# Kernel optimization log

Hardware: AMD Instinct MI355X
Metric: run time of the kernel (lower is better)

## Reference

```python
import jax, jax.numpy as jnp
import numpy as np

NUM_HEADS = 8
NUM_GROUPS = 32
EPS = 1e-5


def group_norm(x, gamma, beta):
    # x: [B, C, H, W]; normalize over (C//G, H, W) within each of G groups
    B, C, H, W = x.shape
    xg = x.reshape(B, NUM_GROUPS, C // NUM_GROUPS, H, W)
    mean = xg.mean(axis=(2, 3, 4), keepdims=True)
    var = xg.var(axis=(2, 3, 4), keepdims=True)
    xn = ((xg - mean) * jax.lax.rsqrt(var + EPS)).reshape(B, C, H, W)
    return xn * gamma[None, :, None, None] + beta[None, :, None, None]


def setup_inputs() -> dict:
    key = jax.random.key(0)
    ks = jax.random.split(key, 7)
    B, C, H, W = 16, 512, 32, 32
    x = jax.random.normal(ks[0], (B, C, H, W), dtype=jnp.float32)
    gamma = jnp.ones((C,), dtype=jnp.float32)
    beta = jnp.zeros((C,), dtype=jnp.float32)
    # 1x1 convs == per-pixel linear layers
    w_qkv = jax.random.normal(ks[1], (3 * C, C), dtype=jnp.float32) * (1.0 / np.sqrt(C))
    b_qkv = jax.random.normal(ks[2], (3 * C,), dtype=jnp.float32) * 0.02
    w_proj = jax.random.normal(ks[3], (C, C), dtype=jnp.float32) * (1.0 / np.sqrt(C))
    b_proj = jax.random.normal(ks[4], (C,), dtype=jnp.float32) * 0.02
    return {"x": x, "gamma": gamma, "beta": beta, "w_qkv": w_qkv,
            "b_qkv": b_qkv, "w_proj": w_proj, "b_proj": b_proj}


def reference(x, gamma, beta, w_qkv, b_qkv, w_proj, b_proj):
    B, C, H, W = x.shape
    nh = NUM_HEADS
    d = C // nh
    N = H * W
    h = group_norm(x, gamma, beta)
    # 1x1 conv: [B,C,H,W] x [3C,C] -> [B,3C,H,W]
    qkv = jnp.einsum('bchw,oc->bohw', h, w_qkv) + b_qkv[None, :, None, None]
    qkv = qkv.reshape(B, 3, nh, d, N)  # matches torch reshape(B,3,heads,d,HW)
    q, k, v = qkv[:, 0], qkv[:, 1], qkv[:, 2]
    scale = d ** (-0.5)
    attn = jnp.einsum('bhdn,bhdm->bhnm', q, k) * scale  # [B,h,N,N]
    attn = jax.nn.softmax(attn, axis=-1)
    out = jnp.einsum('bhnm,bhdm->bhdn', attn, v)  # [B,h,d,N]
    out = out.reshape(B, C, H, W)
    proj = jnp.einsum('bchw,oc->bohw', out, w_proj) + b_proj[None, :, None, None]
    return x + proj
```

## Files before the change

kernel.cpp:

```cpp
#include <hip/hip_runtime.h>
#include <cstddef>

#define B_  16
#define C_  512
#define N_  1024

typedef __attribute__((ext_vector_type(8))) __bf16 bf16x8;
typedef __attribute__((ext_vector_type(4))) float f32x4;
typedef __attribute__((ext_vector_type(4))) short s16x4;

__device__ __forceinline__ unsigned short f2bf(float x) {
  unsigned u = __float_as_uint(x);
  return (unsigned short)((u + 0x7fffu + ((u >> 16) & 1u)) >> 16);
}
__device__ __forceinline__ float bf2f(unsigned short h) {
  return __uint_as_float(((unsigned)h) << 16);
}

#define GLDS16(g, l)                                                            \
  __builtin_amdgcn_global_load_lds(                                             \
      (const __attribute__((address_space(1))) void*)(g),                       \
      (__attribute__((address_space(3))) void*)(l), 16, 0, 0)

__global__ __launch_bounds__(256) void prep_kernel(
    const float* __restrict__ wq, const float* __restrict__ wp,
    unsigned short* __restrict__ oq, unsigned short* __restrict__ op,
    const float* __restrict__ x, float* __restrict__ stats) {
  int tid = threadIdx.x;
  if (blockIdx.x < 1024) {
    int i = blockIdx.x * 256 + tid;
    const float4* src; unsigned short* dst; int off;
    if (i < 196608) { src = (const float4*)wq; dst = oq; off = i; }
    else            { src = (const float4*)wp; dst = op; off = i - 196608; }
    float4 v = src[off];
    union { unsigned short s[4]; ushort4 u; } o;
    o.s[0] = f2bf(v.x); o.s[1] = f2bf(v.y);
    o.s[2] = f2bf(v.z); o.s[3] = f2bf(v.w);
    *(ushort4*)(dst + (size_t)off * 4) = o.u;
    return;
  }
  int bg = blockIdx.x - 1024;
  int b = bg >> 5, g = bg & 31;
  const float4* x4 = (const float4*)(x + ((size_t)b * C_ + (size_t)g * 16) * N_);
  float sum = 0.f, sq = 0.f;
#pragma unroll
  for (int i = 0; i < 16; i++) {
    float4 v = x4[tid + i * 256];
    sum += v.x + v.y + v.z + v.w;
    sq  += v.x * v.x + v.y * v.y + v.z * v.z + v.w * v.w;
  }
#pragma unroll
  for (int off = 32; off > 0; off >>= 1) {
    sum += __shfl_down(sum, off, 64);
    sq  += __shfl_down(sq, off, 64);
  }
  __shared__ float sm[4], sv[4];
  int lane = tid & 63, w = tid >> 6;
  if (lane == 0) { sm[w] = sum; sv[w] = sq; }
  __syncthreads();
  if (tid == 0) {
    float s = sm[0] + sm[1] + sm[2] + sm[3];
    float q = sv[0] + sv[1] + sv[2] + sv[3];
    float mean = s * (1.f / 16384.f);
    float var  = q * (1.f / 16384.f) - mean * mean;
    stats[bg * 2]     = mean;
    stats[bg * 2 + 1] = rsqrtf(var + 1e-5f);
  }
}

__global__ __launch_bounds__(256) void gn_norm(
    const float* __restrict__ x, const float* __restrict__ gamma,
    const float* __restrict__ beta, const float* __restrict__ stats,
    unsigned short* __restrict__ hT) {
  __shared__ __align__(16) unsigned short T[64][72];

  const int bi = blockIdx.x;
  const int nq = bi & 3, g4 = (bi >> 2) & 7, b = bi >> 5;
  const int tid = threadIdx.x, lane = tid & 63, w = tid >> 6;
  const int c0 = g4 * 64, n0 = nq * 256;
  const int q = lane >> 4, n4 = lane & 15;

  const int gidx = b * 32 + g4 * 4 + w;
  const float mean = stats[gidx * 2], rstd = stats[gidx * 2 + 1];
  float ga[4], be[4];
#pragma unroll
  for (int ri = 0; ri < 4; ri++) {
    int c = w * 16 + q + ri * 4;
    ga[ri] = gamma[c0 + c] * rstd;
    be[ri] = beta[c0 + c] - mean * ga[ri];
  }

  const float* xb = x + ((size_t)b * C_ + c0) * N_ + n0;

#pragma unroll
  for (int s = 0; s < 4; s++) {
#pragma unroll
    for (int ri = 0; ri < 4; ri++) {
      int c = w * 16 + q + ri * 4;
      float4 v = *(const float4*)&xb[(size_t)c * N_ + s * 64 + n4 * 4];
      int csw = c ^ ((n4 & 3) << 4);
      T[n4 * 4 + 0][csw] = f2bf(v.x * ga[ri] + be[ri]);
      T[n4 * 4 + 1][csw] = f2bf(v.y * ga[ri] + be[ri]);
      T[n4 * 4 + 2][csw] = f2bf(v.z * ga[ri] + be[ri]);
      T[n4 * 4 + 3][csw] = f2bf(v.w * ga[ri] + be[ri]);
    }
    __syncthreads();
    {
      int n_loc = tid >> 2, cc = (tid & 3) << 4;
      int ccs = cc ^ (((n_loc >> 2) & 3) << 4);
      const uint4* srcp = (const uint4*)&T[n_loc][ccs];
      uint4* dst = (uint4*)&hT[((size_t)b * N_ + n0 + s * 64 + n_loc) * C_ + c0 + cc];
      dst[0] = srcp[0];
      dst[1] = srcp[1];
    }
    __syncthreads();
  }
}

template <int OUT_BF16>
__global__ __launch_bounds__(256) void gemm_mfma(
    const unsigned short* __restrict__ Wb, const float* __restrict__ bias,
    const unsigned short* __restrict__ InT, const float* __restrict__ resid,
    void* __restrict__ Out, int M) {
  __shared__ __align__(16) unsigned short SH[6][128 * 32];

  const int b = blockIdx.z;
  const int n0 = blockIdx.x * 128, m0 = blockIdx.y * 128;
  const int tid = threadIdx.x;
  const int lane = tid & 63, wave = tid >> 6;
  const int col = lane & 15, quad = lane >> 4;
  const int wm = (wave >> 1) << 6, wn = (wave & 1) << 6;

  const unsigned short* Ag = Wb + (size_t)m0 * C_;
  const unsigned short* Bg = InT + ((size_t)b * N_ + n0) * C_;

  const int r0 = tid >> 2, c0 = (tid & 3) << 3;

  auto stage = [&](int buf, int k0) {
    GLDS16(Ag + (size_t)r0 * C_ + k0 + c0,        &SH[buf][tid * 8]);
    GLDS16(Ag + (size_t)(r0 + 64) * C_ + k0 + c0, &SH[buf][(tid + 256) * 8]);
    GLDS16(Bg + (size_t)r0 * C_ + k0 + c0,        &SH[3 + buf][tid * 8]);
    GLDS16(Bg + (size_t)(r0 + 64) * C_ + k0 + c0, &SH[3 + buf][(tid + 256) * 8]);
  };

  f32x4 acc[4][4];
#pragma unroll
  for (int i = 0; i < 4; i++)
#pragma unroll
    for (int j = 0; j < 4; j++) acc[i][j] = f32x4{0.f, 0.f, 0.f, 0.f};

  stage(0, 0);
  stage(1, 32);
  asm volatile("s_waitcnt vmcnt(4)\n\ts_barrier" ::: "memory");

  for (int it = 0; it < 16; it++) {
    const int cur = it % 3;
    if (it < 14) stage((it + 2) % 3, (it + 2) * 32);

    bf16x8 af[4], bfr[4];
#pragma unroll
    for (int mt = 0; mt < 4; mt++)
      af[mt] = *(const bf16x8*)&SH[cur][(wm + mt * 16 + col) * 32 + quad * 8];
#pragma unroll
    for (int nt = 0; nt < 4; nt++)
      bfr[nt] = *(const bf16x8*)&SH[3 + cur][(wn + nt * 16 + col) * 32 + quad * 8];
#pragma unroll
    for (int mt = 0; mt < 4; mt++)
#pragma unroll
      for (int nt = 0; nt < 4; nt++)
        acc[mt][nt] = __builtin_amdgcn_mfma_f32_16x16x32_bf16(
            af[mt], bfr[nt], acc[mt][nt], 0, 0, 0);

    if (it < 14) {
      asm volatile("s_waitcnt vmcnt(4)\n\ts_barrier" ::: "memory");
    } else if (it == 14) {
      asm volatile("s_waitcnt vmcnt(0)\n\ts_barrier" ::: "memory");
    }
  }

  const bool kT = OUT_BF16 && (m0 >= 512) && (m0 < 1024);

  if (kT) {
    unsigned short* epi = &SH[0][0];
    unsigned short* kt_out =
        (unsigned short*)Out + ((size_t)b * 1536 + 512) * N_ + (m0 - 512);
#pragma unroll
    for (int hf = 0; hf < 2; hf++) {
      __syncthreads();
      if ((wave & 1) == hf) {
#pragma unroll
        for (int mt = 0; mt < 4; mt++) {
          int mloc = wm + mt * 16 + quad * 4;
          int mabs = m0 + mloc;
#pragma unroll
          for (int nt = 0; nt < 4; nt++) {
            union { unsigned short s[4]; ushort4 v; } o;
#pragma unroll
            for (int r = 0; r < 4; r++)
              o.s[r] = f2bf(acc[mt][nt][r] + bias[mabs + r]);
            *(ushort4*)&epi[(nt * 16 + col) * 136 + mloc] = o.v;
          }
        }
      }
      __syncthreads();
#pragma unroll
      for (int pass = 0; pass < 4; pass++) {
        int n_l = (tid >> 4) + pass * 16;
        int ch = tid & 15;
        uint4 v = *(const uint4*)&epi[n_l * 136 + ch * 8];
        *(uint4*)(kt_out + (size_t)(n0 + hf * 64 + n_l) * 512 + ch * 8) = v;
      }
    }
    return;
  }

#pragma unroll
  for (int mt = 0; mt < 4; mt++) {
    int mbase = m0 + wm + mt * 16 + quad * 4;
#pragma unroll
    for (int nt = 0; nt < 4; nt++) {
      int n = n0 + wn + nt * 16 + col;
      if constexpr (OUT_BF16) {
#pragma unroll
        for (int r = 0; r < 4; r++) {
          float v = acc[mt][nt][r] + bias[mbase + r];
          ((unsigned short*)Out)[((size_t)b * M + mbase + r) * N_ + n] = f2bf(v);
        }
      } else {
#pragma unroll
        for (int r = 0; r < 4; r++) {
          int m = mbase + r;
          float v = acc[mt][nt][r] + bias[m];
          size_t off = ((size_t)b * M + m) * N_ + n;
          ((float*)Out)[off] = v + resid[off];
        }
      }
    }
  }
}

__device__ __forceinline__ void attn_tile(const bf16x8 (&qf)[2][2],
                                          const bf16x8 (&kf)[4][2],
                                          const s16x4 (&vf)[4][4],
                                          f32x4 (&O)[4][2], float (&l_i)[2]) {
#pragma unroll
  for (int nt = 0; nt < 2; nt++) {
    f32x4 sf[4];
#pragma unroll
    for (int mt = 0; mt < 4; mt++) sf[mt] = f32x4{0.f, 0.f, 0.f, 0.f};
    __builtin_amdgcn_s_setprio(1);
#pragma unroll
    for (int ks = 0; ks < 2; ks++)
#pragma unroll
      for (int mt = 0; mt < 4; mt++)
        sf[mt] = __builtin_amdgcn_mfma_f32_16x16x32_bf16(
            kf[mt][ks], qf[nt][ks], sf[mt], 0, 0, 0);
    __builtin_amdgcn_s_setprio(0);

    s16x4 pb[4];
    float lsum = 0.f;
#pragma unroll
    for (int kc = 0; kc < 4; kc++) {
      float e0 = __expf(sf[kc][0]);
      float e1 = __expf(sf[kc][1]);
      float e2 = __expf(sf[kc][2]);
      float e3 = __expf(sf[kc][3]);
      lsum += (e0 + e1) + (e2 + e3);
      unsigned lo = __builtin_amdgcn_perm(__float_as_uint(e1), __float_as_uint(e0), 0x07060302u);
      unsigned hi = __builtin_amdgcn_perm(__float_as_uint(e3), __float_as_uint(e2), 0x07060302u);
      union { unsigned u[2]; s16x4 v; } t;
      t.u[0] = lo; t.u[1] = hi;
      pb[kc] = t.v;
    }
    l_i[nt] += lsum;

    __builtin_amdgcn_s_setprio(1);
#pragma unroll
    for (int kc = 0; kc < 4; kc++)
#pragma unroll
      for (int mt = 0; mt < 4; mt++)
        O[mt][nt] = __builtin_amdgcn_mfma_f32_16x16x16bf16_1k(
            vf[mt][kc], pb[kc], O[mt][nt], 0, 0, 0);
    __builtin_amdgcn_s_setprio(0);
  }
}

template <int NB, int BOFF>
__global__ __launch_bounds__(256, 2) void attn_mfma(
    const unsigned short* __restrict__ qkv, unsigned short* __restrict__ aoT) {
  __shared__ __align__(16) unsigned short KtL[2][64 * 64];
  __shared__ __align__(16) unsigned short VsL[2][64 * 64];

  const int tid = threadIdx.x;
  const int wave = tid >> 6, lane = tid & 63;
  const int quad = lane >> 4, col = lane & 15;
  const int bi = blockIdx.x;
  const int hh = bi & 7;
  const int bq = bi >> 3;
  const int qb = bq / NB;
  const int b  = BOFF + (bq - qb * NB);
  const int qblk = qb * 128 + wave * 32;

  const unsigned short* qp  = qkv + ((size_t)b * 1536 + hh * 64) * N_;
  const unsigned short* ktp = qkv + ((size_t)b * 1536 + 512) * N_ + hh * 64;
  const unsigned short* vp  = qkv + ((size_t)b * 1536 + 1024 + hh * 64) * N_;

  const int sr = tid >> 3;
  const int sw8 = (((tid & 7) ^ (sr & 7)) << 3);

  bf16x8 qf[2][2];
#pragma unroll
  for (int nt = 0; nt < 2; nt++) {
    int qg = qblk + nt * 16 + col;
#pragma unroll
    for (int ks = 0; ks < 2; ks++) {
      union { unsigned short s[8]; bf16x8 v; } t;
#pragma unroll
      for (int j = 0; j < 8; j++) {
        int d = ks * 32 + quad * 8 + j;
        t.s[j] = f2bf(0.125f * bf2f(qp[(size_t)d * N_ + qg]));
      }
      qf[nt][ks] = t.v;
    }
  }

  float l_i[2];
  f32x4 O[4][2];
#pragma unroll
  for (int nt = 0; nt < 2; nt++) {
    l_i[nt] = 0.f;
#pragma unroll
    for (int mt = 0; mt < 4; mt++) O[mt][nt] = f32x4{0.f, 0.f, 0.f, 0.f};
  }

  {
    const unsigned short* kq = ktp + (size_t)sr * 512 + sw8;
    GLDS16(kq,                    &KtL[0][tid * 8]);
    GLDS16(kq + (size_t)32 * 512, &KtL[0][(256 + tid) * 8]);
    const unsigned short* vq = vp + (size_t)sr * N_ + sw8;
    GLDS16(vq,                    &VsL[0][tid * 8]);
    GLDS16(vq + (size_t)32 * N_,  &VsL[0][(256 + tid) * 8]);
  }
  __syncthreads();

  for (int kt = 0; kt < 16; kt++) {
    const int cur = kt & 1;
    if (kt < 15) {
      const unsigned short* kq = ktp + (size_t)((kt + 1) * 64 + sr) * 512 + sw8;
      GLDS16(kq,                    &KtL[cur ^ 1][tid * 8]);
      GLDS16(kq + (size_t)32 * 512, &KtL[cur ^ 1][(256 + tid) * 8]);
      const unsigned short* vq = vp + (size_t)sr * N_ + (kt + 1) * 64 + sw8;
      GLDS16(vq,                    &VsL[cur ^ 1][tid * 8]);
      GLDS16(vq + (size_t)32 * N_,  &VsL[cur ^ 1][(256 + tid) * 8]);
    }

    bf16x8 kf[4][2];
#pragma unroll
    for (int mt = 0; mt < 4; mt++) {
      int key = 16 * mt + col;
#pragma unroll
      for (int ks = 0; ks < 2; ks++)
        kf[mt][ks] = *(const bf16x8*)
            &KtL[cur][key * 64 + (((ks * 4 + quad) ^ (col & 7)) << 3)];
    }
    s16x4 vf[4][4];
#pragma unroll
    for (int mt = 0; mt < 4; mt++) {
      int d = 16 * mt + col;
#pragma unroll
      for (int kc = 0; kc < 4; kc++)
        vf[mt][kc] = *(const s16x4*)
            &VsL[cur][d * 64 + (((kc * 4 + quad) ^ ((col & 7) << 1)) << 2)];
    }

    attn_tile(qf, kf, vf, O, l_i);

    if (kt < 15) __syncthreads();
  }

#pragma unroll
  for (int nt = 0; nt < 2; nt++) {
    float ls = l_i[nt];
    ls += __shfl_xor(ls, 16, 64);
    ls += __shfl_xor(ls, 32, 64);
    float inv = 1.f / ls;
    int qg = qblk + nt * 16 + col;
    unsigned short* dst = aoT + ((size_t)b * N_ + qg) * C_ + hh * 64;
#pragma unroll
    for (int mt = 0; mt < 4; mt++) {
      union { unsigned short s[4]; ushort4 v; } o;
#pragma unroll
      for (int r = 0; r < 4; r++) o.s[r] = f2bf(O[mt][nt][r] * inv);
      *(ushort4*)(dst + mt * 16 + quad * 4) = o.v;
    }
  }
}

extern "C" void kernel_launch(void* const* d_in, const int* in_sizes, int n_in,
                              void* d_out, int out_size, void* d_ws, size_t ws_size,
                              hipStream_t stream) {
  (void)in_sizes; (void)n_in; (void)out_size; (void)ws_size;
  const float* x      = (const float*)d_in[0];
  const float* gamma  = (const float*)d_in[1];
  const float* beta   = (const float*)d_in[2];
  const float* w_qkv  = (const float*)d_in[3];
  const float* b_qkv  = (const float*)d_in[4];
  const float* w_proj = (const float*)d_in[5];
  const float* b_proj = (const float*)d_in[6];
  float* out = (float*)d_out;

  unsigned short* hT   = (unsigned short*)d_ws;
  unsigned short* qkvb = hT + (size_t)B_ * N_ * C_;
  unsigned short* aoT  = hT;
  unsigned short* wqb  = qkvb + (size_t)B_ * 1536 * N_;
  unsigned short* wpb  = wqb + (size_t)1536 * 512;
  float* stats = (float*)(wpb + (size_t)512 * 512);

  prep_kernel<<<dim3(1024 + 512), dim3(256), 0, stream>>>(w_qkv, w_proj, wqb, wpb, x, stats);
  gn_norm<<<dim3(512), dim3(256), 0, stream>>>(x, gamma, beta, stats, hT);
  gemm_mfma<1><<<dim3(8, 12, 16), dim3(256), 0, stream>>>(
      wqb, b_qkv, hT, (const float*)nullptr, (void*)qkvb, 1536);
  attn_mfma<16, 0><<<dim3(1024), dim3(256), 0, stream>>>(qkvb, aoT);
  gemm_mfma<0><<<dim3(8, 4, 16), dim3(256), 0, stream>>>(
      wpb, b_proj, aoT, x, (void*)out, 512);
}
```

Before: 214.4 us.

## Triple-buffer K/V LDS tiles in attention with partial vmcnt waits

Changes the attention kernel's K/V staging from double to triple buffering. Tiles are now prefetched two iterations ahead, and each barrier waits only until older loads finish (vmcnt(4)) instead of draining all outstanding loads. The aim is to hide more global-to-LDS latency behind MFMA work. In exchange, LDS use per block rises from 32KB to 48KB, which could limit occupancy at 2 blocks per CU, and correctness now depends on hand-written waitcnt counts.

```diff
diff --git a/kernel.cpp b/kernel.cpp
--- a/kernel.cpp
+++ b/kernel.cpp
@@ -288,8 +288,8 @@
 template <int NB, int BOFF>
 __global__ __launch_bounds__(256, 2) void attn_mfma(
     const unsigned short* __restrict__ qkv, unsigned short* __restrict__ aoT) {
-  __shared__ __align__(16) unsigned short KtL[2][64 * 64];
-  __shared__ __align__(16) unsigned short VsL[2][64 * 64];
+  __shared__ __align__(16) unsigned short KtL[3][64 * 64];
+  __shared__ __align__(16) unsigned short VsL[3][64 * 64];
 
   const int tid = threadIdx.x;
   const int wave = tid >> 6, lane = tid & 63;
@@ -308,6 +308,15 @@
   const int sr = tid >> 3;
   const int sw8 = (((tid & 7) ^ (sr & 7)) << 3);
 
+  auto stage = [&](int buf, int kt) {
+    const unsigned short* kq = ktp + (size_t)(kt * 64 + sr) * 512 + sw8;
+    GLDS16(kq,                    &KtL[buf][tid * 8]);
+    GLDS16(kq + (size_t)32 * 512, &KtL[buf][(256 + tid) * 8]);
+    const unsigned short* vq = vp + (size_t)sr * N_ + kt * 64 + sw8;
+    GLDS16(vq,                    &VsL[buf][tid * 8]);
+    GLDS16(vq + (size_t)32 * N_,  &VsL[buf][(256 + tid) * 8]);
+  };
+
   bf16x8 qf[2][2];
 #pragma unroll
   for (int nt = 0; nt < 2; nt++) {
@@ -333,26 +342,13 @@
     for (int mt = 0; mt < 4; mt++) O[mt][nt] = f32x4{0.f, 0.f, 0.f, 0.f};
   }
 
-  {
-    const unsigned short* kq = ktp + (size_t)sr * 512 + sw8;
-    GLDS16(kq,                    &KtL[0][tid * 8]);
-    GLDS16(kq + (size_t)32 * 512, &KtL[0][(256 + tid) * 8]);
-    const unsigned short* vq = vp + (size_t)sr * N_ + sw8;
-    GLDS16(vq,                    &VsL[0][tid * 8]);
-    GLDS16(vq + (size_t)32 * N_,  &VsL[0][(256 + tid) * 8]);
-  }
-  __syncthreads();
+  stage(0, 0);
+  stage(1, 1);
+  asm volatile("s_waitcnt vmcnt(4)\n\ts_barrier" ::: "memory");
 
   for (int kt = 0; kt < 16; kt++) {
-    const int cur = kt & 1;
-    if (kt < 15) {
-      const unsigned short* kq = ktp + (size_t)((kt + 1) * 64 + sr) * 512 + sw8;
-      GLDS16(kq,                    &KtL[cur ^ 1][tid * 8]);
-      GLDS16(kq + (size_t)32 * 512, &KtL[cur ^ 1][(256 + tid) * 8]);
-      const unsigned short* vq = vp + (size_t)sr * N_ + (kt + 1) * 64 + sw8;
-      GLDS16(vq,                    &VsL[cur ^ 1][tid * 8]);
-      GLDS16(vq + (size_t)32 * N_,  &VsL[cur ^ 1][(256 + tid) * 8]);
-    }
+    const int cur = kt % 3;
+    if (kt < 14) stage((kt + 2) % 3, kt + 2);
 
     bf16x8 kf[4][2];
 #pragma unroll
@@ -375,7 +371,11 @@
 
     attn_tile(qf, kf, vf, O, l_i);
 
-    if (kt < 15) __syncthreads();
+    if (kt < 14) {
+      asm volatile("s_waitcnt vmcnt(4)\n\ts_barrier" ::: "memory");
+    } else if (kt == 14) {
+      asm volatile("s_waitcnt vmcnt(0)\n\ts_barrier" ::: "memory");
+    }
   }
 
 #pragma unroll
```

Result: no change. 217.8 us (+1.6%).

## Use 8 waves per attention block, one 16-query tile per wave

Applied to the files above, without the earlier changes.

The attention kernel now runs 512 threads (8 waves) per block instead of 4 waves, and each wave handles one 16-query tile instead of two. Each thread issues one K and one V async LDS load per tile instead of two, and the per-wave register footprint for Q fragments and output accumulators is halved. The aim is more waves to hide latency and a shorter dependency chain per wave. The cost is twice as many waves sharing each K/V tile, so LDS fragment reads are no longer amortised over two query tiles, and block barriers now span more waves.

```diff
diff --git a/kernel.cpp b/kernel.cpp
--- a/kernel.cpp
+++ b/kernel.cpp
@@ -239,54 +239,51 @@
   }
 }
 
-__device__ __forceinline__ void attn_tile(const bf16x8 (&qf)[2][2],
+__device__ __forceinline__ void attn_tile(const bf16x8 (&qf)[2],
                                           const bf16x8 (&kf)[4][2],
                                           const s16x4 (&vf)[4][4],
-                                          f32x4 (&O)[4][2], float (&l_i)[2]) {
-#pragma unroll
-  for (int nt = 0; nt < 2; nt++) {
-    f32x4 sf[4];
-#pragma unroll
-    for (int mt = 0; mt < 4; mt++) sf[mt] = f32x4{0.f, 0.f, 0.f, 0.f};
-    __builtin_amdgcn_s_setprio(1);
-#pragma unroll
-    for (int ks = 0; ks < 2; ks++)
-#pragma unroll
-      for (int mt = 0; mt < 4; mt++)
-        sf[mt] = __builtin_amdgcn_mfma_f32_16x16x32_bf16(
-            kf[mt][ks], qf[nt][ks], sf[mt], 0, 0, 0);
-    __builtin_amdgcn_s_setprio(0);
-
-    s16x4 pb[4];
-    float lsum = 0.f;
-#pragma unroll
-    for (int kc = 0; kc < 4; kc++) {
-      float e0 = __expf(sf[kc][0]);
-      float e1 = __expf(sf[kc][1]);
-      float e2 = __expf(sf[kc][2]);
-      float e3 = __expf(sf[kc][3]);
-      lsum += (e0 + e1) + (e2 + e3);
-      unsigned lo = __builtin_amdgcn_perm(__float_as_uint(e1), __float_as_uint(e0), 0x07060302u);
-      unsigned hi = __builtin_amdgcn_perm(__float_as_uint(e3), __float_as_uint(e2), 0x07060302u);
-      union { unsigned u[2]; s16x4 v; } t;
-      t.u[0] = lo; t.u[1] = hi;
-      pb[kc] = t.v;
-    }
-    l_i[nt] += lsum;
-
-    __builtin_amdgcn_s_setprio(1);
-#pragma unroll
-    for (int kc = 0; kc < 4; kc++)
-#pragma unroll
-      for (int mt = 0; mt < 4; mt++)
-        O[mt][nt] = __builtin_amdgcn_mfma_f32_16x16x16bf16_1k(
-            vf[mt][kc], pb[kc], O[mt][nt], 0, 0, 0);
-    __builtin_amdgcn_s_setprio(0);
-  }
+                                          f32x4 (&O)[4], float& l_i) {
+  f32x4 sf[4];
+#pragma unroll
+  for (int mt = 0; mt < 4; mt++) sf[mt] = f32x4{0.f, 0.f, 0.f, 0.f};
+  __builtin_amdgcn_s_setprio(1);
+#pragma unroll
+  for (int ks = 0; ks < 2; ks++)
+#pragma unroll
+    for (int mt = 0; mt < 4; mt++)
+      sf[mt] = __builtin_amdgcn_mfma_f32_16x16x32_bf16(
+          kf[mt][ks], qf[ks], sf[mt], 0, 0, 0);
+  __builtin_amdgcn_s_setprio(0);
+
+  s16x4 pb[4];
+  float lsum = 0.f;
+#pragma unroll
+  for (int kc = 0; kc < 4; kc++) {
+    float e0 = __expf(sf[kc][0]);
+    float e1 = __expf(sf[kc][1]);
+    float e2 = __expf(sf[kc][2]);
+    float e3 = __expf(sf[kc][3]);
+    lsum += (e0 + e1) + (e2 + e3);
+    unsigned lo = __builtin_amdgcn_perm(__float_as_uint(e1), __float_as_uint(e0), 0x07060302u);
+    unsigned hi = __builtin_amdgcn_perm(__float_as_uint(e3), __float_as_uint(e2), 0x07060302u);
+    union { unsigned u[2]; s16x4 v; } t;
+    t.u[0] = lo; t.u[1] = hi;
+    pb[kc] = t.v;
+  }
+  l_i += lsum;
+
+  __builtin_amdgcn_s_setprio(1);
+#pragma unroll
+  for (int kc = 0; kc < 4; kc++)
+#pragma unroll
+    for (int mt = 0; mt < 4; mt++)
+      O[mt] = __builtin_amdgcn_mfma_f32_16x16x16bf16_1k(
+          vf[mt][kc], pb[kc], O[mt], 0, 0, 0);
+  __builtin_amdgcn_s_setprio(0);
 }
 
 template <int NB, int BOFF>
-__global__ __launch_bounds__(256, 2) void attn_mfma(
+__global__ __launch_bounds__(512, 2) void attn_mfma(
     const unsigned short* __restrict__ qkv, unsigned short* __restrict__ aoT) {
   __shared__ __align__(16) unsigned short KtL[2][64 * 64];
   __shared__ __align__(16) unsigned short VsL[2][64 * 64];
@@ -299,7 +296,7 @@
   const int bq = bi >> 3;
   const int qb = bq / NB;
   const int b  = BOFF + (bq - qb * NB);
-  const int qblk = qb * 128 + wave * 32;
+  const int qg = qb * 128 + wave * 16 + col;
 
   const unsigned short* qp  = qkv + ((size_t)b * 1536 + hh * 64) * N_;
   const unsigned short* ktp = qkv + ((size_t)b * 1536 + 512) * N_ + hh * 64;
@@ -308,50 +305,32 @@
   const int sr = tid >> 3;
   const int sw8 = (((tid & 7) ^ (sr & 7)) << 3);
 
-  bf16x8 qf[2][2];
-#pragma unroll
-  for (int nt = 0; nt < 2; nt++) {
-    int qg = qblk + nt * 16 + col;
-#pragma unroll
-    for (int ks = 0; ks < 2; ks++) {
-      union { unsigned short s[8]; bf16x8 v; } t;
-#pragma unroll
-      for (int j = 0; j < 8; j++) {
-        int d = ks * 32 + quad * 8 + j;
-        t.s[j] = f2bf(0.125f * bf2f(qp[(size_t)d * N_ + qg]));
-      }
-      qf[nt][ks] = t.v;
-    }
-  }
-
-  float l_i[2];
-  f32x4 O[4][2];
-#pragma unroll
-  for (int nt = 0; nt < 2; nt++) {
-    l_i[nt] = 0.f;
-#pragma unroll
-    for (int mt = 0; mt < 4; mt++) O[mt][nt] = f32x4{0.f, 0.f, 0.f, 0.f};
-  }
-
-  {
-    const unsigned short* kq = ktp + (size_t)sr * 512 + sw8;
-    GLDS16(kq,                    &KtL[0][tid * 8]);
-    GLDS16(kq + (size_t)32 * 512, &KtL[0][(256 + tid) * 8]);
-    const unsigned short* vq = vp + (size_t)sr * N_ + sw8;
-    GLDS16(vq,                    &VsL[0][tid * 8]);
-    GLDS16(vq + (size_t)32 * N_,  &VsL[0][(256 + tid) * 8]);
-  }
+  bf16x8 qf[2];
+#pragma unroll
+  for (int ks = 0; ks < 2; ks++) {
+    union { unsigned short s[8]; bf16x8 v; } t;
+#pragma unroll
+    for (int j = 0; j < 8; j++) {
+      int d = ks * 32 + quad * 8 + j;
+      t.s[j] = f2bf(0.125f * bf2f(qp[(size_t)d * N_ + qg]));
+    }
+    qf[ks] = t.v;
+  }
+
+  float l_i = 0.f;
+  f32x4 O[4];
+#pragma unroll
+  for (int mt = 0; mt < 4; mt++) O[mt] = f32x4{0.f, 0.f, 0.f, 0.f};
+
+  GLDS16(ktp + (size_t)sr * 512 + sw8, &KtL[0][tid * 8]);
+  GLDS16(vp + (size_t)sr * N_ + sw8,   &VsL[0][tid * 8]);
   __syncthreads();
 
   for (int kt = 0; kt < 16; kt++) {
     const int cur = kt & 1;
     if (kt < 15) {
-      const unsigned short* kq = ktp + (size_t)((kt + 1) * 64 + sr) * 512 + sw8;
-      GLDS16(kq,                    &KtL[cur ^ 1][tid * 8]);
-      GLDS16(kq + (size_t)32 * 512, &KtL[cur ^ 1][(256 + tid) * 8]);
-      const unsigned short* vq = vp + (size_t)sr * N_ + (kt + 1) * 64 + sw8;
-      GLDS16(vq,                    &VsL[cur ^ 1][tid * 8]);
-      GLDS16(vq + (size_t)32 * N_,  &VsL[cur ^ 1][(256 + tid) * 8]);
+      GLDS16(ktp + (size_t)((kt + 1) * 64 + sr) * 512 + sw8, &KtL[cur ^ 1][tid * 8]);
+      GLDS16(vp + (size_t)sr * N_ + (kt + 1) * 64 + sw8,     &VsL[cur ^ 1][tid * 8]);
     }
 
     bf16x8 kf[4][2];
@@ -378,21 +357,17 @@
     if (kt < 15) __syncthreads();
   }
 
-#pragma unroll
-  for (int nt = 0; nt < 2; nt++) {
-    float ls = l_i[nt];
-    ls += __shfl_xor(ls, 16, 64);
-    ls += __shfl_xor(ls, 32, 64);
-    float inv = 1.f / ls;
-    int qg = qblk + nt * 16 + col;
-    unsigned short* dst = aoT + ((size_t)b * N_ + qg) * C_ + hh * 64;
-#pragma unroll
-    for (int mt = 0; mt < 4; mt++) {
-      union { unsigned short s[4]; ushort4 v; } o;
-#pragma unroll
-      for (int r = 0; r < 4; r++) o.s[r] = f2bf(O[mt][nt][r] * inv);
-      *(ushort4*)(dst + mt * 16 + quad * 4) = o.v;
-    }
+  float ls = l_i;
+  ls += __shfl_xor(ls, 16, 64);
+  ls += __shfl_xor(ls, 32, 64);
+  float inv = 1.f / ls;
+  unsigned short* dst = aoT + ((size_t)b * N_ + qg) * C_ + hh * 64;
+#pragma unroll
+  for (int mt = 0; mt < 4; mt++) {
+    union { unsigned short s[4]; ushort4 v; } o;
+#pragma unroll
+    for (int r = 0; r < 4; r++) o.s[r] = f2bf(O[mt][r] * inv);
+    *(ushort4*)(dst + mt * 16 + quad * 4) = o.v;
   }
 }
 
@@ -420,7 +395,7 @@
   gn_norm<<<dim3(512), dim3(256), 0, stream>>>(x, gamma, beta, stats, hT);
   gemm_mfma<1><<<dim3(8, 12, 16), dim3(256), 0, stream>>>(
       wqb, b_qkv, hT, (const float*)nullptr, (void*)qkvb, 1536);
-  attn_mfma<16, 0><<<dim3(1024), dim3(256), 0, stream>>>(qkvb, aoT);
+  attn_mfma<16, 0><<<dim3(1024), dim3(512), 0, stream>>>(qkvb, aoT);
   gemm_mfma<0><<<dim3(8, 4, 16), dim3(256), 0, stream>>>(
       wpb, b_proj, aoT, x, (void*)out, 512);
 }
```

New measurement: 211.4 us. About the same (-1.4%).
